# Performance work log

Hardware: AMD Instinct MI355X
Metric: run time of the kernel (lower is better)

Reference implementation:

```python
import jax, jax.numpy as jnp
import numpy as np

B, N = 8, 1024
NFEAT, NHID, NHEADS, NCLASS, NLAYERS = 256, 64, 8, 256, 2
ALPHA = 0.2  # LeakyReLU slope inside GAT layers
OUTER_SLOPE = 0.01  # F.leaky_relu default on concatenated heads
NEG = -9e15


def setup_inputs() -> dict:
    key = jax.random.key(0)
    ks = jax.random.split(key, 8)
    x = jax.random.normal(ks[0], (B, N, NFEAT), jnp.float32)
    adj = jax.random.randint(ks[1], (B, N, N), 0, 2).astype(jnp.int32)
    mask = jax.random.randint(ks[2], (B, N), 0, 2).astype(jnp.int32)
    W_att = (jax.random.normal(ks[3], (NHEADS, NFEAT, NHID), jnp.float32) * 0.05)
    a_att = (jax.random.normal(ks[4], (NHEADS, 2 * NHID), jnp.float32) * 0.05)
    W_out = (jax.random.normal(ks[5], (NHID * NHEADS, NCLASS), jnp.float32) * 0.05)
    a_out = (jax.random.normal(ks[6], (2 * NCLASS,), jnp.float32) * 0.05)
    ln_w = jnp.ones((NCLASS,), jnp.float32)
    ln_b = jnp.zeros((NCLASS,), jnp.float32)
    return {"x": x, "adj": adj, "mask": mask, "W_att": W_att, "a_att": a_att,
            "W_out": W_out, "a_out": a_out, "ln_w": ln_w, "ln_b": ln_b}


def _layernorm(x, w, b):
    mu = jnp.mean(x, axis=-1, keepdims=True)
    var = jnp.mean(jnp.square(x - mu), axis=-1, keepdims=True)
    return (x - mu) * jax.lax.rsqrt(var + 1e-5) * w + b


def _gat_forward(x, adj_pos, maskb, W_att, a_att, W_out, a_out, ln_w, ln_b):
    for _ in range(NLAYERS):
        # multi-head GAT layers (concat=True): e_ij = leakyrelu(f1_i + f2_j)
        h = jnp.einsum('bnf,hfo->bhno', x, W_att)            # [B,H,N,F]
        f1 = jnp.einsum('bhno,ho->bhn', h, a_att[:, :NHID])  # [B,H,N]
        f2 = jnp.einsum('bhno,ho->bhn', h, a_att[:, NHID:])
        e = jax.nn.leaky_relu(f1[:, :, :, None] + f2[:, :, None, :], ALPHA)
        att = jax.nn.softmax(jnp.where(adj_pos[:, None], e, NEG), axis=-1)
        hp = jax.nn.elu(jnp.einsum('bhnm,bhmo->bhno', att, h))
        y = jax.nn.leaky_relu(
            hp.transpose(0, 2, 1, 3).reshape(B, N, NHEADS * NHID), OUTER_SLOPE)
        # out attention layer (concat=False)
        ho = y @ W_out                                        # [B,N,C]
        g1 = ho @ a_out[:NCLASS]                              # [B,N]
        g2 = ho @ a_out[NCLASS:]
        eo = jax.nn.leaky_relu(g1[:, :, None] + g2[:, None, :], ALPHA)
        ao = jax.nn.softmax(jnp.where(adj_pos, eo, NEG), axis=-1)
        x = x + jax.nn.elu(jnp.einsum('bnm,bmo->bno', ao, ho))
        x = jnp.where(maskb, 0.0, x)
        x = _layernorm(x, ln_w, ln_b)
    return jax.nn.relu(x), jax.nn.relu(x[:, 0, :])


def reference(x, adj, mask, W_att, a_att, W_out, a_out, ln_w, ln_b):
    adj_pos = adj > 0
    maskb = (mask == 0)[:, :, None]
    return _gat_forward(x, adj_pos, maskb, W_att, a_att, W_out, a_out, ln_w, ln_b)
```

## Files before the change

kernel.cpp:

```cpp
#include <hip/hip_runtime.h>
#include <hip/hip_bf16.h>
#include <math.h>

#define BB 8
#define NN 1024
#define FF 256
#define HH 8
#define OO 64
#define CC 256

typedef __attribute__((ext_vector_type(8))) short short8;
typedef __attribute__((ext_vector_type(4))) short s16x4;
typedef __attribute__((ext_vector_type(4))) float f32x4;
typedef unsigned long long u64;

__device__ __forceinline__ short bf16s(float f) {
    __hip_bfloat16 h = __float2bfloat16(f);
    return *reinterpret_cast<short*>(&h);
}

__global__ void k_xprep(const float* __restrict__ x, __hip_bfloat16* __restrict__ xbf) {
    int i = blockIdx.x * 256 + threadIdx.x;
    xbf[i] = __float2bfloat16(x[i]);
}

__global__ void k_adjprep(const int* __restrict__ adj, u64* __restrict__ adjbit) {
    int i = blockIdx.x * 256 + threadIdx.x;
    u64 m = __ballot(adj[i] > 0);
    if ((threadIdx.x & 63) == 0) adjbit[i >> 6] = m;
}

__global__ void k_wprep(const float* __restrict__ Wa, const float* __restrict__ Wo,
                        __hip_bfloat16* __restrict__ WaT, __hip_bfloat16* __restrict__ WoT) {
    int i = blockIdx.x * 256 + threadIdx.x;
    if (i < 131072) {
        int hd = i >> 14, o = (i >> 8) & 63, f = i & 255;
        WaT[i] = __float2bfloat16(Wa[hd * 16384 + f * 64 + o]);
    } else {
        int j = i - 131072;
        int c = j >> 9, k = j & 511;
        WoT[j] = __float2bfloat16(Wo[k * 256 + c]);
    }
}

__global__ void k_proj_mfma(const __hip_bfloat16* __restrict__ xbf,
                            const __hip_bfloat16* __restrict__ WaT,
                            const float* __restrict__ aatt,
                            __hip_bfloat16* __restrict__ hF,
                            float* __restrict__ f1, float* __restrict__ f2) {
    int tile = blockIdx.x, hd = blockIdx.y;
    int t = threadIdx.x, lane = t & 63, w = t >> 6;
    int r0 = tile * 64;
    int b = r0 >> 10;
    int n0 = r0 & 1023;
    int bh = b * HH + hd;
    int al = lane & 15, ah = lane >> 4;
    const __hip_bfloat16* xrow = xbf + (size_t)(r0 + w * 16 + al) * FF;
    const __hip_bfloat16* Wb = WaT + (size_t)hd * OO * FF;
    f32x4 z4 = {0.f, 0.f, 0.f, 0.f};
    f32x4 acc[4] = {z4, z4, z4, z4};
    for (int k0 = 0; k0 < FF; k0 += 32) {
        int k = k0 + ah * 8;
        short8 af = *(const short8*)&xrow[k];
#pragma unroll
        for (int cf = 0; cf < 4; ++cf) {
            int col = cf * 16 + al;
            short8 bf = *(const short8*)&Wb[(size_t)col * FF + k];
            acc[cf] = __builtin_amdgcn_mfma_f32_16x16x32_bf16(af, bf, acc[cf], 0, 0, 0);
        }
    }
    int kw = tile & 15;
    int half = w >> 1;
    int hg = (w & 1) * 2 + (ah >> 1);
    int q0 = (ah & 1) * 4;
#pragma unroll
    for (int cf = 0; cf < 4; ++cf) {
        size_t base = ((((size_t)bh * 16 + kw) * 4 + cf) * 2 + half) * 512 +
                      (hg * 16 + al) * 8 + q0;
        s16x4 v;
#pragma unroll
        for (int r = 0; r < 4; ++r) v[r] = bf16s(acc[cf][r]);
        *(s16x4*)&hF[base] = v;
    }
    int nb = n0 + w * 16 + ah * 4;
    float p1[4] = {0.f, 0.f, 0.f, 0.f}, p2[4] = {0.f, 0.f, 0.f, 0.f};
#pragma unroll
    for (int cf = 0; cf < 4; ++cf) {
        int col = cf * 16 + al;
        float a1 = aatt[hd * 2 * OO + col];
        float a2 = aatt[hd * 2 * OO + OO + col];
#pragma unroll
        for (int r = 0; r < 4; ++r) {
            p1[r] += acc[cf][r] * a1;
            p2[r] += acc[cf][r] * a2;
        }
    }
#pragma unroll
    for (int off = 1; off < 16; off <<= 1) {
#pragma unroll
        for (int r = 0; r < 4; ++r) {
            p1[r] += __shfl_xor(p1[r], off);
            p2[r] += __shfl_xor(p2[r], off);
        }
    }
    if (al == 0) {
#pragma unroll
        for (int r = 0; r < 4; ++r) {
            f1[(size_t)bh * NN + nb + r] = p1[r];
            f2[(size_t)bh * NN + nb + r] = p2[r];
        }
    }
}

__global__ void k_att_fused(const u64* __restrict__ adjbit, const float* __restrict__ f1,
                            const float* __restrict__ f2,
                            const __hip_bfloat16* __restrict__ hF,
                            __hip_bfloat16* __restrict__ ybf) {
    int orig = blockIdx.x;
    int wgid = (orig & 7) * 128 + (orig >> 3);
    int bh = wgid >> 4;
    int n0 = (wgid & 15) * 64;
    int b = bh >> 3, hd = bh & 7;
    int t = threadIdx.x, lane = t & 63, w = t >> 6;
    __shared__ float Qs[1024], Ss[1024];
    __shared__ u64 bits[64 * 17];
    const float* f2b = f2 + (size_t)bh * NN;
    for (int j = t; j < 1024; j += 256) {
        float v = f2b[j];
        Qs[j] = __expf(v);
        Ss[j] = __expf(0.2f * v);
    }
    for (int e = t; e < 1024; e += 256) {
        int rr = e >> 4, c = e & 15;
        bits[rr * 17 + c] = adjbit[((size_t)b * NN + n0 + rr) * 16 + c];
    }
    int g = lane >> 4, r = lane & 15;
    int row = w * 16 + r;
    float fl = f1[(size_t)bh * NN + n0 + row];
    float P = __expf(fl), R = __expf(0.2f * fl);
    __syncthreads();
    const __hip_bfloat16* hFb = hF + (size_t)bh * 16 * 4 * 2 * 512 + lane * 8;
    f32x4 z4 = {0.f, 0.f, 0.f, 0.f};
    f32x4 acc[4] = {z4, z4, z4, z4};
    float ps = 0.f;
    int c0 = g * 8;
#pragma unroll 2
    for (int k0 = 0; k0 < NN; k0 += 64) {
        int kw = k0 >> 6;
        u64 m = bits[row * 17 + kw];
        unsigned bl0 = (unsigned)(m >> c0) & 0xffu;
        unsigned bl1 = (unsigned)(m >> (32 + c0)) & 0xffu;
        f32x4 qa0 = *(const f32x4*)&Qs[k0 + c0];
        f32x4 qb0 = *(const f32x4*)&Qs[k0 + c0 + 4];
        f32x4 sa0 = *(const f32x4*)&Ss[k0 + c0];
        f32x4 sb0 = *(const f32x4*)&Ss[k0 + c0 + 4];
        f32x4 qa1 = *(const f32x4*)&Qs[k0 + 32 + c0];
        f32x4 qb1 = *(const f32x4*)&Qs[k0 + 32 + c0 + 4];
        f32x4 sa1 = *(const f32x4*)&Ss[k0 + 32 + c0];
        f32x4 sb1 = *(const f32x4*)&Ss[k0 + 32 + c0 + 4];
        short8 a0, a1;
#pragma unroll
        for (int e = 0; e < 4; ++e) {
            float v0 = ((bl0 >> e) & 1) ? fmaxf(P * qa0[e], R * sa0[e]) : 0.f;
            float v1 = ((bl0 >> (4 + e)) & 1) ? fmaxf(P * qb0[e], R * sb0[e]) : 0.f;
            float v2 = ((bl1 >> e) & 1) ? fmaxf(P * qa1[e], R * sa1[e]) : 0.f;
            float v3 = ((bl1 >> (4 + e)) & 1) ? fmaxf(P * qb1[e], R * sb1[e]) : 0.f;
            ps += (v0 + v1) + (v2 + v3);
            a0[e] = bf16s(v0);
            a0[4 + e] = bf16s(v1);
            a1[e] = bf16s(v2);
            a1[4 + e] = bf16s(v3);
        }
#pragma unroll
        for (int cf = 0; cf < 4; ++cf) {
            const __hip_bfloat16* blk = hFb + ((size_t)(kw * 4 + cf) * 2) * 512;
            short8 b0 = *(const short8*)&blk[0];
            short8 b1 = *(const short8*)&blk[512];
            acc[cf] = __builtin_amdgcn_mfma_f32_16x16x32_bf16(a0, b0, acc[cf], 0, 0, 0);
            acc[cf] = __builtin_amdgcn_mfma_f32_16x16x32_bf16(a1, b1, acc[cf], 0, 0, 0);
        }
    }
    ps += __shfl_xor(ps, 16);
    ps += __shfl_xor(ps, 32);
#pragma unroll
    for (int rr = 0; rr < 4; ++rr) {
        int rloc = g * 4 + rr;
        float dn = __shfl(ps, rloc);
        float ids = 1.0f / dn;
        int nrow = n0 + w * 16 + rloc;
#pragma unroll
        for (int cf = 0; cf < 4; ++cf) {
            float v = acc[cf][rr] * ids;
            float e = v > 0.f ? v : expm1f(v);
            float yv = e > 0.f ? e : 0.01f * e;
            ybf[((size_t)b * NN + nrow) * 512 + hd * OO + cf * 16 + r] =
                __float2bfloat16(yv);
        }
    }
}

__global__ void k_outproj_mfma(const __hip_bfloat16* __restrict__ ybf,
                               const __hip_bfloat16* __restrict__ WoT,
                               const float* __restrict__ ao,
                               __hip_bfloat16* __restrict__ hoF,
                               float* __restrict__ g1, float* __restrict__ g2) {
    int tile = blockIdx.x;
    int t = threadIdx.x, lane = t & 63, w = t >> 6;
    int r0 = tile * 32;
    int b = r0 >> 10;
    __shared__ __align__(16) __hip_bfloat16 As[32][520];
    __shared__ float pg1[4][32], pg2[4][32];
    for (int e = t; e < 2048; e += 256) {
        int row = e >> 6, k8 = (e & 63) * 8;
        *(short8*)&As[row][k8] = *(const short8*)&ybf[(size_t)(r0 + row) * 512 + k8];
    }
    __syncthreads();
    int al = lane & 15, ah = lane >> 4;
    f32x4 z4 = {0.f, 0.f, 0.f, 0.f};
    f32x4 acc0[4] = {z4, z4, z4, z4};
    f32x4 acc1[4] = {z4, z4, z4, z4};
    for (int k0 = 0; k0 < 512; k0 += 32) {
        int k = k0 + ah * 8;
        short8 a0 = *(const short8*)&As[al][k];
        short8 a1 = *(const short8*)&As[16 + al][k];
#pragma unroll
        for (int cf = 0; cf < 4; ++cf) {
            int col = w * 64 + cf * 16 + al;
            short8 bf = *(const short8*)&WoT[(size_t)col * 512 + k];
            acc0[cf] = __builtin_amdgcn_mfma_f32_16x16x32_bf16(a0, bf, acc0[cf], 0, 0, 0);
            acc1[cf] = __builtin_amdgcn_mfma_f32_16x16x32_bf16(a1, bf, acc1[cf], 0, 0, 0);
        }
    }
    int kw = (tile >> 1) & 15;
    int half = tile & 1;
    int hg0 = ah >> 1;
    int q0 = (ah & 1) * 4;
    float q1[8] = {0.f, 0.f, 0.f, 0.f, 0.f, 0.f, 0.f, 0.f};
    float q2[8] = {0.f, 0.f, 0.f, 0.f, 0.f, 0.f, 0.f, 0.f};
#pragma unroll
    for (int cf = 0; cf < 4; ++cf) {
        int col = w * 64 + cf * 16 + al;
        int cfB = w * 4 + cf;
        float a1v = ao[col], a2v = ao[CC + col];
        size_t base = ((((size_t)b * 16 + kw) * 16 + cfB) * 2 + half) * 512;
        s16x4 v0, v1;
#pragma unroll
        for (int r = 0; r < 4; ++r) {
            v0[r] = bf16s(acc0[cf][r]);
            v1[r] = bf16s(acc1[cf][r]);
            q1[r] += acc0[cf][r] * a1v;
            q2[r] += acc0[cf][r] * a2v;
            q1[4 + r] += acc1[cf][r] * a1v;
            q2[4 + r] += acc1[cf][r] * a2v;
        }
        *(s16x4*)&hoF[base + (hg0 * 16 + al) * 8 + q0] = v0;
        *(s16x4*)&hoF[base + ((hg0 + 2) * 16 + al) * 8 + q0] = v1;
    }
#pragma unroll
    for (int off = 1; off < 16; off <<= 1) {
#pragma unroll
        for (int j = 0; j < 8; ++j) {
            q1[j] += __shfl_xor(q1[j], off);
            q2[j] += __shfl_xor(q2[j], off);
        }
    }
    if (al == 0) {
#pragma unroll
        for (int j = 0; j < 8; ++j) {
            int row = (j >> 2) * 16 + ah * 4 + (j & 3);
            pg1[w][row] = q1[j];
            pg2[w][row] = q2[j];
        }
    }
    __syncthreads();
    if (t < 32) {
        g1[r0 + t] = pg1[0][t] + pg1[1][t] + pg1[2][t] + pg1[3][t];
        g2[r0 + t] = pg2[0][t] + pg2[1][t] + pg2[2][t] + pg2[3][t];
    }
}

__global__ void k_out_fused(const u64* __restrict__ adjbit, const float* __restrict__ g1,
                            const float* __restrict__ g2,
                            const __hip_bfloat16* __restrict__ hoF,
                            const float* __restrict__ xin, const int* __restrict__ mask,
                            const float* __restrict__ lw, const float* __restrict__ lb,
                            float* __restrict__ xout, __hip_bfloat16* __restrict__ xbfout,
                            float* __restrict__ outf, int final_) {
    int orig = blockIdx.x;
    int wgid = (orig & 7) * 64 + (orig >> 3);
    int b = wgid >> 6;
    int n0 = (wgid & 63) * 16;
    int t = threadIdx.x, lane = t & 63, w = t >> 6;
    __shared__ float Qs[1024], Ss[1024];
    __shared__ u64 bits[16 * 17];
    __shared__ __align__(16) __hip_bfloat16 As[16][264];
    __shared__ float psum[4][16];
    __shared__ float lns[4][16], lnq[4][16];
    const float* g2b = g2 + (size_t)b * NN;
    for (int j = t; j < 1024; j += 256) {
        float v = g2b[j];
        Qs[j] = __expf(v);
        Ss[j] = __expf(0.2f * v);
    }
    {
        int rr = t >> 4, c = t & 15;
        bits[rr * 17 + c] = adjbit[((size_t)b * NN + n0 + rr) * 16 + c];
    }
    int br = t & 15, kg = t >> 4;
    float gl = g1[(size_t)b * NN + n0 + br];
    float P = __expf(gl);
    float R = __expf(0.2f * gl);
    int ar = lane & 15, g = lane >> 4;
    const __hip_bfloat16* hoFb = hoF + (size_t)b * 16 * 16 * 2 * 512 + lane * 8;
    f32x4 z4 = {0.f, 0.f, 0.f, 0.f};
    f32x4 acc[4] = {z4, z4, z4, z4};
    float ps = 0.f;
    __syncthreads();
    for (int ks = 0; ks < NN; ks += 256) {
        u64 m = bits[br * 17 + (ks >> 6) + (kg >> 2)];
        int sh = (kg & 3) * 16;
        short8 vv[2];
#pragma unroll
        for (int h = 0; h < 2; ++h) {
            short8 vx;
#pragma unroll
            for (int e4 = 0; e4 < 2; ++e4) {
                int cw = kg * 16 + h * 8 + e4 * 4;
                f32x4 q4 = *(const f32x4*)&Qs[ks + cw];
                f32x4 s4 = *(const f32x4*)&Ss[ks + cw];
#pragma unroll
                for (int e = 0; e < 4; ++e) {
                    float val = ((m >> (sh + h * 8 + e4 * 4 + e)) & 1)
                                    ? fmaxf(P * q4[e], R * s4[e]) : 0.f;
                    ps += val;
                    vx[e4 * 4 + e] = bf16s(val);
                }
            }
            vv[h] = vx;
        }
        *(short8*)&As[br][kg * 16] = vv[0];
        *(short8*)&As[br][kg * 16 + 8] = vv[1];
        __syncthreads();
#pragma unroll
        for (int ksub = 0; ksub < 4; ++ksub) {
            int kw = (ks >> 6) + ksub;
            short8 a0 = *(const short8*)&As[ar][ksub * 64 + g * 8];
            short8 a1 = *(const short8*)&As[ar][ksub * 64 + 32 + g * 8];
#pragma unroll
            for (int cf = 0; cf < 4; ++cf) {
                int cfB = w * 4 + cf;
                const __hip_bfloat16* blk = hoFb + ((size_t)(kw * 16 + cfB) * 2) * 512;
                short8 b0 = *(const short8*)&blk[0];
                short8 b1 = *(const short8*)&blk[512];
                acc[cf] = __builtin_amdgcn_mfma_f32_16x16x32_bf16(a0, b0, acc[cf], 0, 0, 0);
                acc[cf] = __builtin_amdgcn_mfma_f32_16x16x32_bf16(a1, b1, acc[cf], 0, 0, 0);
            }
        }
        __syncthreads();
    }
    ps += __shfl_xor(ps, 16);
    ps += __shfl_xor(ps, 32);
    if (lane < 16) psum[w][lane] = ps;
    __syncthreads();
    float tv[4][4];
#pragma unroll
    for (int rr = 0; rr < 4; ++rr) {
        int rloc = g * 4 + rr;
        float dn = psum[0][rloc] + psum[1][rloc] + psum[2][rloc] + psum[3][rloc];
        float ids = 1.0f / dn;
        int nrow = n0 + rloc;
        int mk = mask[b * NN + nrow];
        size_t rowo = ((size_t)b * NN + nrow) * CC;
        float s1 = 0.f, s2 = 0.f;
#pragma unroll
        for (int cf = 0; cf < 4; ++cf) {
            int col = w * 64 + cf * 16 + ar;
            float v = acc[cf][rr] * ids;
            float e = v > 0.f ? v : expm1f(v);
            float tvv = (mk == 0) ? 0.f : (xin[rowo + col] + e);
            tv[rr][cf] = tvv;
            s1 += tvv;
            s2 += tvv * tvv;
        }
#pragma unroll
        for (int off = 1; off < 16; off <<= 1) {
            s1 += __shfl_xor(s1, off);
            s2 += __shfl_xor(s2, off);
        }
        if (ar == 0) {
            lns[w][rloc] = s1;
            lnq[w][rloc] = s2;
        }
    }
    __syncthreads();
#pragma unroll
    for (int rr = 0; rr < 4; ++rr) {
        int rloc = g * 4 + rr;
        int nrow = n0 + rloc;
        size_t rowo = ((size_t)b * NN + nrow) * CC;
        float su = lns[0][rloc] + lns[1][rloc] + lns[2][rloc] + lns[3][rloc];
        float sq = lnq[0][rloc] + lnq[1][rloc] + lnq[2][rloc] + lnq[3][rloc];
        float mu = su * (1.0f / CC);
        float var = sq * (1.0f / CC) - mu * mu;
        float rstd = rsqrtf(var + 1e-5f);
#pragma unroll
        for (int cf = 0; cf < 4; ++cf) {
            int col = w * 64 + cf * 16 + ar;
            float ln = (tv[rr][cf] - mu) * rstd * lw[col] + lb[col];
            if (final_) {
                float rv = ln > 0.f ? ln : 0.f;
                outf[rowo + col] = rv;
                if (nrow == 0) outf[(size_t)BB * NN * CC + b * CC + col] = rv;
            } else {
                xout[rowo + col] = ln;
                xbfout[rowo + col] = __float2bfloat16(ln);
            }
        }
    }
}

extern "C" void kernel_launch(void* const* d_in, const int* in_sizes, int n_in,
                              void* d_out, int out_size, void* d_ws, size_t ws_size,
                              hipStream_t stream) {
    const float* x = (const float*)d_in[0];
    const int* adj = (const int*)d_in[1];
    const int* mask = (const int*)d_in[2];
    const float* W_att = (const float*)d_in[3];
    const float* a_att = (const float*)d_in[4];
    const float* W_out = (const float*)d_in[5];
    const float* a_out = (const float*)d_in[6];
    const float* ln_w = (const float*)d_in[7];
    const float* ln_b = (const float*)d_in[8];
    float* out = (float*)d_out;

    float* ws = (float*)d_ws;
    float* xbuf = ws;
    float* xbfr = xbuf + 2097152;
    float* f1   = xbfr + 2097152;
    float* f2   = f1 + 65536;
    float* g1   = f2 + 65536;
    float* g2   = g1 + 8192;
    float* p    = g2 + 8192;
    __hip_bfloat16* xbf = (__hip_bfloat16*)xbfr;
    __hip_bfloat16* hF  = (__hip_bfloat16*)p;
    __hip_bfloat16* ybf = (__hip_bfloat16*)(p + 2097152);
    __hip_bfloat16* hoF = (__hip_bfloat16*)(p + 4194304);
    __hip_bfloat16* WaT = (__hip_bfloat16*)(p + 5242880);
    __hip_bfloat16* WoT = (__hip_bfloat16*)(p + 5308416);
    u64* adjbit = (u64*)(p + 5373952);

    k_wprep<<<1024, 256, 0, stream>>>(W_att, W_out, WaT, WoT);
    k_adjprep<<<32768, 256, 0, stream>>>(adj, adjbit);
    k_xprep<<<8192, 256, 0, stream>>>(x, xbf);

    for (int layer = 0; layer < 2; ++layer) {
        const float* xin_l = layer ? xbuf : x;
        k_proj_mfma<<<dim3(128, 8), 256, 0, stream>>>(xbf, WaT, a_att, hF, f1, f2);
        k_att_fused<<<1024, 256, 0, stream>>>(adjbit, f1, f2, hF, ybf);
        k_outproj_mfma<<<256, 256, 0, stream>>>(ybf, WoT, a_out, hoF, g1, g2);
        k_out_fused<<<512, 256, 0, stream>>>(adjbit, g1, g2, hoF, xin_l, mask,
                                             ln_w, ln_b, xbuf, xbf, out, layer == 1);
    }
}
```

Before: 226.4 us.

## Compute attention A-fragments in registers and merge prep kernels into one launch

In the output-attention kernel, each wave now builds its own bf16 attention fragments directly in the MFMA register layout instead of writing them to a shared tile. This removes the shared As buffer and the two barriers per 256-column step. Row sums are taken with a wave shuffle instead of a shared psum reduction. The cost is that all four waves recompute the same exp/select work, four times the ALU work for that part. The three preprocessing kernels are also merged into one launch to cut launch overhead.

```diff
diff --git a/kernel.cpp b/kernel.cpp
--- a/kernel.cpp
+++ b/kernel.cpp
@@ -19,27 +19,28 @@
     return *reinterpret_cast<short*>(&h);
 }
 
-__global__ void k_xprep(const float* __restrict__ x, __hip_bfloat16* __restrict__ xbf) {
-    int i = blockIdx.x * 256 + threadIdx.x;
-    xbf[i] = __float2bfloat16(x[i]);
-}
-
-__global__ void k_adjprep(const int* __restrict__ adj, u64* __restrict__ adjbit) {
-    int i = blockIdx.x * 256 + threadIdx.x;
-    u64 m = __ballot(adj[i] > 0);
-    if ((threadIdx.x & 63) == 0) adjbit[i >> 6] = m;
-}
-
-__global__ void k_wprep(const float* __restrict__ Wa, const float* __restrict__ Wo,
-                        __hip_bfloat16* __restrict__ WaT, __hip_bfloat16* __restrict__ WoT) {
-    int i = blockIdx.x * 256 + threadIdx.x;
-    if (i < 131072) {
-        int hd = i >> 14, o = (i >> 8) & 63, f = i & 255;
-        WaT[i] = __float2bfloat16(Wa[hd * 16384 + f * 64 + o]);
+__global__ void k_prep(const int* __restrict__ adj, const float* __restrict__ x,
+                       const float* __restrict__ Wa, const float* __restrict__ Wo,
+                       u64* __restrict__ adjbit, __hip_bfloat16* __restrict__ xbf,
+                       __hip_bfloat16* __restrict__ WaT, __hip_bfloat16* __restrict__ WoT) {
+    int bid = blockIdx.x, t = threadIdx.x;
+    if (bid < 32768) {
+        int i = bid * 256 + t;
+        u64 m = __ballot(adj[i] > 0);
+        if ((t & 63) == 0) adjbit[i >> 6] = m;
+    } else if (bid < 32768 + 8192) {
+        int i = (bid - 32768) * 256 + t;
+        xbf[i] = __float2bfloat16(x[i]);
     } else {
-        int j = i - 131072;
-        int c = j >> 9, k = j & 511;
-        WoT[j] = __float2bfloat16(Wo[k * 256 + c]);
+        int i = (bid - 32768 - 8192) * 256 + t;
+        if (i < 131072) {
+            int hd = i >> 14, o = (i >> 8) & 63, f = i & 255;
+            WaT[i] = __float2bfloat16(Wa[hd * 16384 + f * 64 + o]);
+        } else {
+            int j = i - 131072;
+            int c = j >> 9, k = j & 511;
+            WoT[j] = __float2bfloat16(Wo[k * 256 + c]);
+        }
     }
 }
 
@@ -293,8 +294,6 @@
     int t = threadIdx.x, lane = t & 63, w = t >> 6;
     __shared__ float Qs[1024], Ss[1024];
     __shared__ u64 bits[16 * 17];
-    __shared__ __align__(16) __hip_bfloat16 As[16][264];
-    __shared__ float psum[4][16];
     __shared__ float lns[4][16], lnq[4][16];
     const float* g2b = g2 + (size_t)b * NN;
     for (int j = t; j < 1024; j += 256) {
@@ -302,71 +301,64 @@
         Qs[j] = __expf(v);
         Ss[j] = __expf(0.2f * v);
     }
-    {
+    if (t < 256) {
         int rr = t >> 4, c = t & 15;
         bits[rr * 17 + c] = adjbit[((size_t)b * NN + n0 + rr) * 16 + c];
     }
-    int br = t & 15, kg = t >> 4;
-    float gl = g1[(size_t)b * NN + n0 + br];
+    int g = lane >> 4, r = lane & 15;
+    float gl = g1[(size_t)b * NN + n0 + r];
     float P = __expf(gl);
     float R = __expf(0.2f * gl);
-    int ar = lane & 15, g = lane >> 4;
+    __syncthreads();
     const __hip_bfloat16* hoFb = hoF + (size_t)b * 16 * 16 * 2 * 512 + lane * 8;
     f32x4 z4 = {0.f, 0.f, 0.f, 0.f};
     f32x4 acc[4] = {z4, z4, z4, z4};
     float ps = 0.f;
-    __syncthreads();
-    for (int ks = 0; ks < NN; ks += 256) {
-        u64 m = bits[br * 17 + (ks >> 6) + (kg >> 2)];
-        int sh = (kg & 3) * 16;
-        short8 vv[2];
-#pragma unroll
-        for (int h = 0; h < 2; ++h) {
-            short8 vx;
-#pragma unroll
-            for (int e4 = 0; e4 < 2; ++e4) {
-                int cw = kg * 16 + h * 8 + e4 * 4;
-                f32x4 q4 = *(const f32x4*)&Qs[ks + cw];
-                f32x4 s4 = *(const f32x4*)&Ss[ks + cw];
-#pragma unroll
-                for (int e = 0; e < 4; ++e) {
-                    float val = ((m >> (sh + h * 8 + e4 * 4 + e)) & 1)
-                                    ? fmaxf(P * q4[e], R * s4[e]) : 0.f;
-                    ps += val;
-                    vx[e4 * 4 + e] = bf16s(val);
-                }
-            }
-            vv[h] = vx;
-        }
-        *(short8*)&As[br][kg * 16] = vv[0];
-        *(short8*)&As[br][kg * 16 + 8] = vv[1];
-        __syncthreads();
-#pragma unroll
-        for (int ksub = 0; ksub < 4; ++ksub) {
-            int kw = (ks >> 6) + ksub;
-            short8 a0 = *(const short8*)&As[ar][ksub * 64 + g * 8];
-            short8 a1 = *(const short8*)&As[ar][ksub * 64 + 32 + g * 8];
-#pragma unroll
-            for (int cf = 0; cf < 4; ++cf) {
-                int cfB = w * 4 + cf;
-                const __hip_bfloat16* blk = hoFb + ((size_t)(kw * 16 + cfB) * 2) * 512;
-                short8 b0 = *(const short8*)&blk[0];
-                short8 b1 = *(const short8*)&blk[512];
-                acc[cf] = __builtin_amdgcn_mfma_f32_16x16x32_bf16(a0, b0, acc[cf], 0, 0, 0);
-                acc[cf] = __builtin_amdgcn_mfma_f32_16x16x32_bf16(a1, b1, acc[cf], 0, 0, 0);
-            }
-        }
-        __syncthreads();
+    int c0 = g * 8;
+#pragma unroll 2
+    for (int k0 = 0; k0 < NN; k0 += 64) {
+        int kw = k0 >> 6;
+        u64 m = bits[r * 17 + kw];
+        unsigned bl0 = (unsigned)(m >> c0) & 0xffu;
+        unsigned bl1 = (unsigned)(m >> (32 + c0)) & 0xffu;
+        f32x4 qa0 = *(const f32x4*)&Qs[k0 + c0];
+        f32x4 qb0 = *(const f32x4*)&Qs[k0 + c0 + 4];
+        f32x4 sa0 = *(const f32x4*)&Ss[k0 + c0];
+        f32x4 sb0 = *(const f32x4*)&Ss[k0 + c0 + 4];
+        f32x4 qa1 = *(const f32x4*)&Qs[k0 + 32 + c0];
+        f32x4 qb1 = *(const f32x4*)&Qs[k0 + 32 + c0 + 4];
+        f32x4 sa1 = *(const f32x4*)&Ss[k0 + 32 + c0];
+        f32x4 sb1 = *(const f32x4*)&Ss[k0 + 32 + c0 + 4];
+        short8 a0, a1;
+#pragma unroll
+        for (int e = 0; e < 4; ++e) {
+            float v0 = ((bl0 >> e) & 1) ? fmaxf(P * qa0[e], R * sa0[e]) : 0.f;
+            float v1 = ((bl0 >> (4 + e)) & 1) ? fmaxf(P * qb0[e], R * sb0[e]) : 0.f;
+            float v2 = ((bl1 >> e) & 1) ? fmaxf(P * qa1[e], R * sa1[e]) : 0.f;
+            float v3 = ((bl1 >> (4 + e)) & 1) ? fmaxf(P * qb1[e], R * sb1[e]) : 0.f;
+            ps += (v0 + v1) + (v2 + v3);
+            a0[e] = bf16s(v0);
+            a0[4 + e] = bf16s(v1);
+            a1[e] = bf16s(v2);
+            a1[4 + e] = bf16s(v3);
+        }
+#pragma unroll
+        for (int cf = 0; cf < 4; ++cf) {
+            int cfB = w * 4 + cf;
+            const __hip_bfloat16* blk = hoFb + ((size_t)(kw * 16 + cfB) * 2) * 512;
+            short8 b0 = *(const short8*)&blk[0];
+            short8 b1 = *(const short8*)&blk[512];
+            acc[cf] = __builtin_amdgcn_mfma_f32_16x16x32_bf16(a0, b0, acc[cf], 0, 0, 0);
+            acc[cf] = __builtin_amdgcn_mfma_f32_16x16x32_bf16(a1, b1, acc[cf], 0, 0, 0);
+        }
     }
     ps += __shfl_xor(ps, 16);
     ps += __shfl_xor(ps, 32);
-    if (lane < 16) psum[w][lane] = ps;
-    __syncthreads();
     float tv[4][4];
 #pragma unroll
     for (int rr = 0; rr < 4; ++rr) {
         int rloc = g * 4 + rr;
-        float dn = psum[0][rloc] + psum[1][rloc] + psum[2][rloc] + psum[3][rloc];
+        float dn = __shfl(ps, rloc);
         float ids = 1.0f / dn;
         int nrow = n0 + rloc;
         int mk = mask[b * NN + nrow];
@@ -374,7 +366,7 @@
         float s1 = 0.f, s2 = 0.f;
 #pragma unroll
         for (int cf = 0; cf < 4; ++cf) {
-            int col = w * 64 + cf * 16 + ar;
+            int col = w * 64 + cf * 16 + r;
             float v = acc[cf][rr] * ids;
             float e = v > 0.f ? v : expm1f(v);
             float tvv = (mk == 0) ? 0.f : (xin[rowo + col] + e);
@@ -387,7 +379,7 @@
             s1 += __shfl_xor(s1, off);
             s2 += __shfl_xor(s2, off);
         }
-        if (ar == 0) {
+        if (r == 0) {
             lns[w][rloc] = s1;
             lnq[w][rloc] = s2;
         }
@@ -405,7 +397,7 @@
         float rstd = rsqrtf(var + 1e-5f);
 #pragma unroll
         for (int cf = 0; cf < 4; ++cf) {
-            int col = w * 64 + cf * 16 + ar;
+            int col = w * 64 + cf * 16 + r;
             float ln = (tv[rr][cf] - mu) * rstd * lw[col] + lb[col];
             if (final_) {
                 float rv = ln > 0.f ? ln : 0.f;
@@ -449,9 +441,8 @@
     __hip_bfloat16* WoT = (__hip_bfloat16*)(p + 5308416);
     u64* adjbit = (u64*)(p + 5373952);
 
-    k_wprep<<<1024, 256, 0, stream>>>(W_att, W_out, WaT, WoT);
-    k_adjprep<<<32768, 256, 0, stream>>>(adj, adjbit);
-    k_xprep<<<8192, 256, 0, stream>>>(x, xbf);
+    k_prep<<<32768 + 8192 + 1024, 256, 0, stream>>>(adj, x, W_att, W_out,
+                                                    adjbit, xbf, WaT, WoT);
 
     for (int layer = 0; layer < 2; ++layer) {
         const float* xin_l = layer ? xbuf : x;
```

After: 224.5 us. Within noise of the previous version (-0.8%).
